# Kernel optimization log

Measured on AMD Instinct MI355X. Metric: run time of the kernel, lower is better.

The kernel has to match this reference:

```python
import jax, jax.numpy as jnp
import numpy as np

# --- hyperparameters (match module defaults) ---
W_CLASSIFY = 1.1          # weight_factor_classify
W_SAMPLE = 1.0            # weight_factor_sample (mid weight add)
LOSS_WEIGHTS = (1.0, 1.0, 1.0)
PARAMS_HEAD = dict(a=80.0, b=1500.0, c=1750.0, d=2000.0, t=-0.5)
PARAMS_CHEST = dict(a=10.0, b=75.0, c=85.0, d=100.0, t=-0.5)
PARAMS_NECK = dict(a=0.15, b=1.5, c=1.7, d=1.9, t=-0.5)

# AIS thresholds (reimplemented in-kernel; original used numpy round-trips)
HEAD_THR = np.array([150.0, 500.0, 1000.0, 1800.0, 2600.0], dtype=np.float32)
CHEST_THR = np.array([22.0, 35.0, 45.0, 55.0, 65.0], dtype=np.float32)
CHEST_OT_SCALE = np.array([0.8, 0.9, 1.0, 1.1, 1.2], dtype=np.float32)  # per occupant-type
NECK_THR = np.array([0.2, 0.5, 1.0, 1.5, 2.0], dtype=np.float32)


def piecewise_linear(y_true, y_pred, p, mid):
    a, b, c, d, t = p['a'], p['b'], p['c'], p['d'], p['t']
    k = -np.log(t + 1.0) / d  # decay rate for y > d
    w = jnp.zeros_like(y_true)
    w = jnp.where((y_true >= 0) & (y_true < a), (mid / a) * y_true, w)
    w = jnp.where((y_true >= a) & (y_true <= b), mid, w)
    w = jnp.where((y_true > b) & (y_true < c), mid - (mid / (c - b)) * (y_true - b), w)
    w = jnp.where((y_true >= c) & (y_true <= d), 0.0, w)
    w = jnp.where(y_true > d, -1.0 + jnp.exp(-k * (y_true - d)), w)
    w = w + jnp.where(y_pred < 0, mid, 0.0)
    return w


def ais_from_thresholds(x, thr):
    # piecewise-constant AIS class: number of thresholds exceeded, in [0, 5]
    return jnp.sum(x[:, None] >= thr[None, :], axis=-1).astype(jnp.float32)


def task_loss(pred, true, ais_pred, ais_true, params):
    # AIS values are classification results of detached values in the
    # original (no grad) -> stop_gradient here.
    w_cls = W_CLASSIFY ** jnp.abs(jax.lax.stop_gradient(ais_pred) - jax.lax.stop_gradient(ais_true))
    w_mid = 1.0 + piecewise_linear(true, pred, params, W_SAMPLE)
    base = jnp.abs(pred - true)  # MAE, reduction='none'
    return jnp.mean(base * w_cls * w_mid)


def setup_inputs() -> dict:
    key = jax.random.key(0)
    k1, k2, k3 = jax.random.split(key, 3)
    B = 4194304
    scales = jnp.array([2500.0, 120.0, 2.5], dtype=jnp.float32)  # HIC, Dmax, Nij ranges
    pred = (jax.random.uniform(k1, (B, 3), dtype=jnp.float32) * 1.1 - 0.05) * scales
    true = jax.random.uniform(k2, (B, 3), dtype=jnp.float32) * scales
    ot = jax.random.randint(k3, (B,), 0, 5, dtype=jnp.int32)
    return {"pred": pred, "true": true, "ot": ot}


def reference(pred, true, ot):
    thr_head = jnp.asarray(HEAD_THR)
    thr_neck = jnp.asarray(NECK_THR)
    # chest thresholds scale with occupant type -> per-sample thresholds
    thr_chest = jnp.asarray(CHEST_THR)[None, :] * jnp.asarray(CHEST_OT_SCALE)[ot][:, None]

    p_hic, p_dmax, p_nij = pred[:, 0], pred[:, 1], pred[:, 2]
    t_hic, t_dmax, t_nij = true[:, 0], true[:, 1], true[:, 2]

    loss_hic = task_loss(p_hic, t_hic,
                         ais_from_thresholds(p_hic, thr_head),
                         ais_from_thresholds(t_hic, thr_head), PARAMS_HEAD)

    ais_p_chest = jnp.sum(p_dmax[:, None] >= thr_chest, axis=-1).astype(jnp.float32)
    ais_t_chest = jnp.sum(t_dmax[:, None] >= thr_chest, axis=-1).astype(jnp.float32)
    loss_dmax = task_loss(p_dmax, t_dmax, ais_p_chest, ais_t_chest, PARAMS_CHEST)

    loss_nij = task_loss(p_nij, t_nij,
                         ais_from_thresholds(p_nij, thr_neck),
                         ais_from_thresholds(t_nij, thr_neck), PARAMS_NECK)

    w_hic, w_dmax, w_nij = LOSS_WEIGHTS
    return w_hic * loss_hic + w_dmax * loss_dmax + w_nij * loss_nij
```

## Files before the change

kernel.cpp:

```cpp
#include <hip/hip_runtime.h>

#define NBLOCKS 1024
#define NTHREADS 256

__device__ __forceinline__ float wmid(float yt, float yp,
                                      float a, float b, float c, float d) {
    float w;
    if (yt < 0.0f)       w = 0.0f;
    else if (yt < a)     w = yt * (1.0f / a);
    else if (yt <= b)    w = 1.0f;
    else if (yt < c)     w = 1.0f - (yt - b) * (1.0f / (c - b));
    else if (yt <= d)    w = 0.0f;
    else                 w = -1.0f + exp2f(-(yt - d) * (1.0f / d));
    if (yp < 0.0f) w += 1.0f;
    return 1.0f + w;
}

__device__ __forceinline__ float row_loss(float ph, float pd, float pn,
                                          float th, float td, float tn, int ot) {
    const float L2_11 = 0.13750352374993502f;

    int ap = (ph >= 150.0f) + (ph >= 500.0f) + (ph >= 1000.0f) + (ph >= 1800.0f) + (ph >= 2600.0f);
    int at = (th >= 150.0f) + (th >= 500.0f) + (th >= 1000.0f) + (th >= 1800.0f) + (th >= 2600.0f);
    float wc = exp2f(fabsf((float)(ap - at)) * L2_11);
    float l  = fabsf(ph - th) * wc * wmid(th, ph, 80.0f, 1500.0f, 1750.0f, 2000.0f);

    float s = 0.8f + 0.1f * (float)ot;
    ap = (pd >= 22.0f*s) + (pd >= 35.0f*s) + (pd >= 45.0f*s) + (pd >= 55.0f*s) + (pd >= 65.0f*s);
    at = (td >= 22.0f*s) + (td >= 35.0f*s) + (td >= 45.0f*s) + (td >= 55.0f*s) + (td >= 65.0f*s);
    wc = exp2f(fabsf((float)(ap - at)) * L2_11);
    l += fabsf(pd - td) * wc * wmid(td, pd, 10.0f, 75.0f, 85.0f, 100.0f);

    ap = (pn >= 0.2f) + (pn >= 0.5f) + (pn >= 1.0f) + (pn >= 1.5f) + (pn >= 2.0f);
    at = (tn >= 0.2f) + (tn >= 0.5f) + (tn >= 1.0f) + (tn >= 1.5f) + (tn >= 2.0f);
    wc = exp2f(fabsf((float)(ap - at)) * L2_11);
    l += fabsf(pn - tn) * wc * wmid(tn, pn, 0.15f, 1.5f, 1.7f, 1.9f);

    return l;
}

__global__ __launch_bounds__(NTHREADS)
void weighted_loss_main(const float* __restrict__ pred,
                        const float* __restrict__ truth,
                        const int*   __restrict__ ot,
                        float* __restrict__ partial, int B) {
    const int nq     = B >> 2;
    const int gid    = blockIdx.x * blockDim.x + threadIdx.x;
    const int stride = gridDim.x * blockDim.x;
    const float4* p4 = (const float4*)pred;
    const float4* t4 = (const float4*)truth;
    const int4*   o4 = (const int4*)ot;

    float acc = 0.0f;
    for (int q = gid; q < nq; q += stride) {
        float4 pa = p4[3*q + 0], pb = p4[3*q + 1], pc = p4[3*q + 2];
        float4 ta = t4[3*q + 0], tb = t4[3*q + 1], tc = t4[3*q + 2];
        int4   o  = o4[q];
        float ph[4] = {pa.x, pa.w, pb.z, pc.y};
        float pD[4] = {pa.y, pb.x, pb.w, pc.z};
        float pn[4] = {pa.z, pb.y, pc.x, pc.w};
        float th[4] = {ta.x, ta.w, tb.z, tc.y};
        float tD[4] = {ta.y, tb.x, tb.w, tc.z};
        float tn[4] = {ta.z, tb.y, tc.x, tc.w};
        int   oo[4] = {o.x, o.y, o.z, o.w};
        #pragma unroll
        for (int j = 0; j < 4; ++j)
            acc += row_loss(ph[j], pD[j], pn[j], th[j], tD[j], tn[j], oo[j]);
    }
    for (int r = (nq << 2) + gid; r < B; r += stride)
        acc += row_loss(pred[3*r], pred[3*r+1], pred[3*r+2],
                        truth[3*r], truth[3*r+1], truth[3*r+2], ot[r]);

    #pragma unroll
    for (int off = 32; off > 0; off >>= 1) acc += __shfl_down(acc, off, 64);
    __shared__ float sm[NTHREADS / 64];
    const int lane = threadIdx.x & 63, wid = threadIdx.x >> 6;
    if (lane == 0) sm[wid] = acc;
    __syncthreads();
    if (threadIdx.x == 0) {
        float s = 0.0f;
        #pragma unroll
        for (int w = 0; w < NTHREADS / 64; ++w) s += sm[w];
        partial[blockIdx.x] = s;
    }
}

__global__ __launch_bounds__(256)
void weighted_loss_reduce(const float* __restrict__ partial, int n,
                          float* __restrict__ out, float invB) {
    float acc = 0.0f;
    for (int i = threadIdx.x; i < n; i += blockDim.x) acc += partial[i];
    #pragma unroll
    for (int off = 32; off > 0; off >>= 1) acc += __shfl_down(acc, off, 64);
    __shared__ float sm[4];
    const int lane = threadIdx.x & 63, wid = threadIdx.x >> 6;
    if (lane == 0) sm[wid] = acc;
    __syncthreads();
    if (threadIdx.x == 0)
        out[0] = (sm[0] + sm[1] + sm[2] + sm[3]) * invB;
}

extern "C" void kernel_launch(void* const* d_in, const int* in_sizes, int n_in,
                              void* d_out, int out_size, void* d_ws, size_t ws_size,
                              hipStream_t stream) {
    const float* pred  = (const float*)d_in[0];
    const float* truth = (const float*)d_in[1];
    const int*   ot    = (const int*)d_in[2];
    const int B = in_sizes[2];
    float* partial = (float*)d_ws;

    weighted_loss_main<<<NBLOCKS, NTHREADS, 0, stream>>>(pred, truth, ot, partial, B);
    weighted_loss_reduce<<<1, 256, 0, stream>>>(partial, NBLOCKS, (float*)d_out,
                                                1.0f / (float)B);
}
```

Measured before the change: 143.4 us.

## Process flattened float4 chunks with per-thread fixed roles and branchless weights

```diff
diff --git a/kernel.cpp b/kernel.cpp
--- a/kernel.cpp
+++ b/kernel.cpp
@@ -1,86 +1,117 @@
 #include <hip/hip_runtime.h>
 
-#define NBLOCKS 1024
-#define NTHREADS 256
+#define NT 256
+#define NB 1536
 
-__device__ __forceinline__ float wmid(float yt, float yp,
-                                      float a, float b, float c, float d) {
-    float w;
-    if (yt < 0.0f)       w = 0.0f;
-    else if (yt < a)     w = yt * (1.0f / a);
-    else if (yt <= b)    w = 1.0f;
-    else if (yt < c)     w = 1.0f - (yt - b) * (1.0f / (c - b));
-    else if (yt <= d)    w = 0.0f;
-    else                 w = -1.0f + exp2f(-(yt - d) * (1.0f / d));
-    if (yp < 0.0f) w += 1.0f;
-    return 1.0f + w;
+__device__ __forceinline__ float elem_loss(float p, float t, float se,
+    float t0, float t1, float t2, float t3, float t4,
+    float ainv, float bb, float cbinv, float dd, float dinv) {
+    float u0 = t0 * se, u1 = t1 * se, u2 = t2 * se, u3 = t3 * se, u4 = t4 * se;
+    int ap = (p >= u0) + (p >= u1) + (p >= u2) + (p >= u3) + (p >= u4);
+    int at = (t >= u0) + (t >= u1) + (t >= u2) + (t >= u3) + (t >= u4);
+    float wc = exp2f(fabsf((float)(ap - at)) * 0.13750352374993502f);
+    float ramp = t * ainv;
+    float down = 1.0f - (t - bb) * cbinv;
+    float wm = fmaxf(fminf(fminf(ramp, 1.0f), down), 0.0f);
+    float tail = exp2f((dd - t) * dinv) - 1.0f;
+    wm = (t > dd) ? tail : wm;
+    wm += (p < 0.0f) ? 2.0f : 1.0f;
+    return fabsf(p - t) * wc * wm;
 }
 
-__device__ __forceinline__ float row_loss(float ph, float pd, float pn,
-                                          float th, float td, float tn, int ot) {
-    const float L2_11 = 0.13750352374993502f;
+#define SEL0(x0, x1, x2) (c1 ? (x1) : (c2 ? (x2) : (x0)))
+#define SEL1(x0, x1, x2) (c1 ? (x2) : (c2 ? (x0) : (x1)))
+#define SEL2(x0, x1, x2) (c1 ? (x0) : (c2 ? (x1) : (x2)))
 
-    int ap = (ph >= 150.0f) + (ph >= 500.0f) + (ph >= 1000.0f) + (ph >= 1800.0f) + (ph >= 2600.0f);
-    int at = (th >= 150.0f) + (th >= 500.0f) + (th >= 1000.0f) + (th >= 1800.0f) + (th >= 2600.0f);
-    float wc = exp2f(fabsf((float)(ap - at)) * L2_11);
-    float l  = fabsf(ph - th) * wc * wmid(th, ph, 80.0f, 1500.0f, 1750.0f, 2000.0f);
+#define DECL_SLOT(n, SEL) \
+    const float t0_##n = SEL(150.0f, 22.0f, 0.2f); \
+    const float t1_##n = SEL(500.0f, 35.0f, 0.5f); \
+    const float t2_##n = SEL(1000.0f, 45.0f, 1.0f); \
+    const float t3_##n = SEL(1800.0f, 55.0f, 1.5f); \
+    const float t4_##n = SEL(2600.0f, 65.0f, 2.0f); \
+    const float ainv_##n = SEL(0.0125f, 0.1f, 6.6666667f); \
+    const float bb_##n   = SEL(1500.0f, 75.0f, 1.5f); \
+    const float cbinv_##n= SEL(0.004f, 0.1f, 5.0f); \
+    const float dd_##n   = SEL(2000.0f, 100.0f, 1.9f); \
+    const float dinv_##n = SEL(0.0005f, 0.01f, 0.52631579f); \
+    const bool  ch_##n   = SEL(false, true, false);
 
-    float s = 0.8f + 0.1f * (float)ot;
-    ap = (pd >= 22.0f*s) + (pd >= 35.0f*s) + (pd >= 45.0f*s) + (pd >= 55.0f*s) + (pd >= 65.0f*s);
-    at = (td >= 22.0f*s) + (td >= 35.0f*s) + (td >= 45.0f*s) + (td >= 55.0f*s) + (td >= 65.0f*s);
-    wc = exp2f(fabsf((float)(ap - at)) * L2_11);
-    l += fabsf(pd - td) * wc * wmid(td, pd, 10.0f, 75.0f, 85.0f, 100.0f);
+#define SLOT_LOSS(n, p, t) \
+    elem_loss((p), (t), ch_##n ? (off_##n ? s1 : s0) : 1.0f, \
+              t0_##n, t1_##n, t2_##n, t3_##n, t4_##n, \
+              ainv_##n, bb_##n, cbinv_##n, dd_##n, dinv_##n)
 
-    ap = (pn >= 0.2f) + (pn >= 0.5f) + (pn >= 1.0f) + (pn >= 1.5f) + (pn >= 2.0f);
-    at = (tn >= 0.2f) + (tn >= 0.5f) + (tn >= 1.0f) + (tn >= 1.5f) + (tn >= 2.0f);
-    wc = exp2f(fabsf((float)(ap - at)) * L2_11);
-    l += fabsf(pn - tn) * wc * wmid(tn, pn, 0.15f, 1.5f, 1.7f, 1.9f);
-
-    return l;
-}
-
-__global__ __launch_bounds__(NTHREADS)
+__global__ __launch_bounds__(NT)
 void weighted_loss_main(const float* __restrict__ pred,
                         const float* __restrict__ truth,
                         const int*   __restrict__ ot,
                         float* __restrict__ partial, int B) {
-    const int nq     = B >> 2;
-    const int gid    = blockIdx.x * blockDim.x + threadIdx.x;
-    const int stride = gridDim.x * blockDim.x;
+    const int total  = 3 * B;
+    const int nchunk = total >> 2;
+    const int g = blockIdx.x * NT + threadIdx.x;
+    const int S = gridDim.x * NT;
+
+    const int  q  = g % 3;
+    const bool c1 = (q == 1), c2 = (q == 2);
+
+    DECL_SLOT(a, SEL0)
+    DECL_SLOT(b, SEL1)
+    DECL_SLOT(c, SEL2)
+
+    const bool off_a = false;
+    const bool off_b = c2;
+    const bool off_c = c1 || c2;
+    const bool off_d = true;
+
     const float4* p4 = (const float4*)pred;
     const float4* t4 = (const float4*)truth;
-    const int4*   o4 = (const int4*)ot;
 
     float acc = 0.0f;
-    for (int q = gid; q < nq; q += stride) {
-        float4 pa = p4[3*q + 0], pb = p4[3*q + 1], pc = p4[3*q + 2];
-        float4 ta = t4[3*q + 0], tb = t4[3*q + 1], tc = t4[3*q + 2];
-        int4   o  = o4[q];
-        float ph[4] = {pa.x, pa.w, pb.z, pc.y};
-        float pD[4] = {pa.y, pb.x, pb.w, pc.z};
-        float pn[4] = {pa.z, pb.y, pc.x, pc.w};
-        float th[4] = {ta.x, ta.w, tb.z, tc.y};
-        float tD[4] = {ta.y, tb.x, tb.w, tc.z};
-        float tn[4] = {ta.z, tb.y, tc.x, tc.w};
-        int   oo[4] = {o.x, o.y, o.z, o.w};
-        #pragma unroll
-        for (int j = 0; j < 4; ++j)
-            acc += row_loss(ph[j], pD[j], pn[j], th[j], tD[j], tn[j], oo[j]);
+    for (int C = g; C < nchunk; C += S) {
+        float4 pv = p4[C];
+        float4 tv = t4[C];
+        unsigned r0 = (unsigned)(((4u * (unsigned)C - (unsigned)q) * 0xAAAAAAABull) >> 33);
+        int o0 = ot[r0];
+        int o1 = ot[r0 + 1];
+        float s0 = fmaf(0.1f, (float)o0, 0.8f);
+        float s1 = fmaf(0.1f, (float)o1, 0.8f);
+
+        acc += SLOT_LOSS(a, pv.x, tv.x);
+        acc += SLOT_LOSS(b, pv.y, tv.y);
+        acc += SLOT_LOSS(c, pv.z, tv.z);
+        acc += elem_loss(pv.w, tv.w, ch_a ? (off_d ? s1 : s0) : 1.0f,
+                         t0_a, t1_a, t2_a, t3_a, t4_a,
+                         ainv_a, bb_a, cbinv_a, dd_a, dinv_a);
+        (void)off_a;
     }
-    for (int r = (nq << 2) + gid; r < B; r += stride)
-        acc += row_loss(pred[3*r], pred[3*r+1], pred[3*r+2],
-                        truth[3*r], truth[3*r+1], truth[3*r+2], ot[r]);
+
+    for (int idx = (nchunk << 2) + g; idx < total; idx += S) {
+        int role = idx % 3, row = idx / 3;
+        float p = pred[idx], t = truth[idx];
+        float l;
+        if (role == 0)
+            l = elem_loss(p, t, 1.0f, 150.0f, 500.0f, 1000.0f, 1800.0f, 2600.0f,
+                          0.0125f, 1500.0f, 0.004f, 2000.0f, 0.0005f);
+        else if (role == 1)
+            l = elem_loss(p, t, fmaf(0.1f, (float)ot[row], 0.8f),
+                          22.0f, 35.0f, 45.0f, 55.0f, 65.0f,
+                          0.1f, 75.0f, 0.1f, 100.0f, 0.01f);
+        else
+            l = elem_loss(p, t, 1.0f, 0.2f, 0.5f, 1.0f, 1.5f, 2.0f,
+                          6.6666667f, 1.5f, 5.0f, 1.9f, 0.52631579f);
+        acc += l;
+    }
 
     #pragma unroll
     for (int off = 32; off > 0; off >>= 1) acc += __shfl_down(acc, off, 64);
-    __shared__ float sm[NTHREADS / 64];
+    __shared__ float sm[NT / 64];
     const int lane = threadIdx.x & 63, wid = threadIdx.x >> 6;
     if (lane == 0) sm[wid] = acc;
     __syncthreads();
     if (threadIdx.x == 0) {
         float s = 0.0f;
         #pragma unroll
-        for (int w = 0; w < NTHREADS / 64; ++w) s += sm[w];
+        for (int w = 0; w < NT / 64; ++w) s += sm[w];
         partial[blockIdx.x] = s;
     }
 }
@@ -109,7 +140,7 @@
     const int B = in_sizes[2];
     float* partial = (float*)d_ws;
 
-    weighted_loss_main<<<NBLOCKS, NTHREADS, 0, stream>>>(pred, truth, ot, partial, B);
-    weighted_loss_reduce<<<1, 256, 0, stream>>>(partial, NBLOCKS, (float*)d_out,
+    weighted_loss_main<<<NB, NT, 0, stream>>>(pred, truth, ot, partial, B);
+    weighted_loss_reduce<<<1, 256, 0, stream>>>(partial, NB, (float*)d_out,
                                                 1.0f / (float)B);
 }
```

After: 138.4 us. 3.5% less time.
